# Kernel optimization log

Measured on AMD Instinct MI355X. Metric: run time of the kernel, lower is better.

## Reference

```python
import jax, jax.numpy as jnp
import numpy as np

B, T, N, D = 8, 512, 64, 128
PRED, HEADS, HID = 96, 8, 256
KERNELS = (17, 49)
NUM_LAYERS = 1
NUM_BLOCKS = 1
IDX_T = np.arange(64)   # lowest 64 of T//2=256 rfft modes (mode_select='low')
IDX_C = np.arange(32)   # min(modes, (N+1)//2)=32 lowest channel-frequency modes


def _mov_avg(x, k):
    # x: [B, T, N]; replicate-pad (k-1)//2 on both ends, then box filter (AvgPool1d stride 1)
    pad = (k - 1) // 2
    xp = jnp.concatenate([jnp.repeat(x[:, :1], pad, axis=1), x, jnp.repeat(x[:, -1:], pad, axis=1)], axis=1)
    c = jnp.cumsum(xp, axis=1)
    c = jnp.concatenate([jnp.zeros_like(c[:, :1]), c], axis=1)
    return (c[:, k:] - c[:, :-k]) / k


def _decomp_multi(x, dec_w, dec_b):
    # series_decomp_multi: softmax-weighted mixture of moving averages
    mm = jnp.stack([_mov_avg(x, k) for k in KERNELS], axis=-1)        # [B,T,N,K]
    w = jax.nn.softmax(x[..., None] * dec_w + dec_b, axis=-1)         # Linear(1,K) on x, softmax over K
    trend = jnp.sum(mm * w, axis=-1)
    return x - trend, trend


def _complex_attn(x, Wq, Wk, Wv, Wo):
    # x: complex64 [B, L, M, D]; multi-head attention over the M selected frequency modes.
    # Real projection weights applied to complex activations; attention weights are
    # softmax over |q k^H| / sqrt(dh); values stay complex.
    Bq, L, M, Dm = x.shape
    dh = Dm // HEADS
    q = jnp.einsum('blmd,de->blme', x, Wq).reshape(Bq, L, M, HEADS, dh)
    k = jnp.einsum('blmd,de->blme', x, Wk).reshape(Bq, L, M, HEADS, dh)
    v = jnp.einsum('blmd,de->blme', x, Wv).reshape(Bq, L, M, HEADS, dh)
    s = jnp.einsum('blmhd,blnhd->blhmn', q, jnp.conj(k))              # complex scores
    w = jax.nn.softmax(jnp.abs(s) / np.sqrt(dh), axis=-1)             # real attn weights
    o = jnp.einsum('blhmn,blnhd->blmhd', w.astype(x.dtype), v).reshape(Bq, L, M, Dm)
    return jnp.einsum('blmd,de->blme', o, Wo)


def _cem(x, Wq, Wk, Wv, Wo):
    # channel-frequency attention; x: [B, N, T, D]
    xp = jnp.transpose(x, (0, 2, 1, 3))                               # [B,T,N,D]
    xf = jnp.fft.rfft(xp, axis=2)                                     # [B,T,N//2+1,D]
    xs = xf[:, :, IDX_C, :]                                           # gather selected modes
    for _ in range(NUM_LAYERS):
        xs = _complex_attn(xs, Wq, Wk, Wv, Wo)
    yf = jnp.zeros((x.shape[0], T, N // 2 + 1, D), dtype=xf.dtype).at[:, :, IDX_C, :].set(xs)
    y = jnp.fft.irfft(yf, n=N, axis=2)
    return jnp.transpose(y, (0, 2, 1, 3))


def _tem(x, Wq, Wk, Wv, Wo):
    # temporal-frequency attention; x: [B, N, T, D]
    xf = jnp.fft.rfft(x, axis=2)                                      # [B,N,T//2+1,D]
    xs = xf[:, :, IDX_T, :]
    for _ in range(NUM_LAYERS):
        xs = _complex_attn(xs, Wq, Wk, Wv, Wo)
    yf = jnp.zeros((x.shape[0], N, T // 2 + 1, D), dtype=xf.dtype).at[:, :, IDX_T, :].set(xs)
    return jnp.fft.irfft(yf, n=T, axis=2)


def setup_inputs() -> dict:
    key = jax.random.key(0)
    ks = jax.random.split(key, 24)
    r = lambda i, shape, s: jax.random.normal(ks[i], shape, jnp.float32) * s
    K = len(KERNELS)
    return {
        'x': jax.random.normal(ks[0], (B, T, N), jnp.float32),
        'embeddings': jax.random.normal(ks[1], (1, D), jnp.float32),
        'dec_w': r(2, (K,), 1.0),
        'dec_b': jnp.zeros((K,), jnp.float32),
        'mlp_w1': r(3, (T, HID), 1.0 / np.sqrt(T)),
        'mlp_b1': jnp.zeros((HID,), jnp.float32),
        'mlp_w2': r(4, (HID, HID), 1.0 / np.sqrt(HID)),
        'mlp_b2': jnp.zeros((HID,), jnp.float32),
        'mlp_w3': r(5, (HID, PRED), 1.0 / np.sqrt(HID)),
        'mlp_b3': jnp.zeros((PRED,), jnp.float32),
        'cem_Wq': r(6, (D, D), 0.02), 'cem_Wk': r(7, (D, D), 0.02),
        'cem_Wv': r(8, (D, D), 0.02), 'cem_Wo': r(9, (D, D), 0.02),
        'tem_Wq': r(10, (D, D), 0.02), 'tem_Wk': r(11, (D, D), 0.02),
        'tem_Wv': r(12, (D, D), 0.02), 'tem_Wo': r(13, (D, D), 0.02),
        'dr_w': r(14, (D, 1), 1.0 / np.sqrt(D)),
        'dr_b': jnp.zeros((1,), jnp.float32),
        'out_w': r(15, (T, PRED), 1.0 / np.sqrt(T)),
        'out_b': jnp.zeros((PRED,), jnp.float32),
        'W_fuse': jnp.ones((2,), jnp.float32),
    }


def reference(x, embeddings, dec_w, dec_b, mlp_w1, mlp_b1, mlp_w2, mlp_b2, mlp_w3, mlp_b3,
              cem_Wq, cem_Wk, cem_Wv, cem_Wo, tem_Wq, tem_Wk, tem_Wv, tem_Wo,
              dr_w, dr_b, out_w, out_b, W_fuse):
    res, trend = _decomp_multi(x, dec_w, dec_b)
    t = jnp.transpose(trend, (0, 2, 1))                               # [B,N,T]
    h = jax.nn.relu(t @ mlp_w1 + mlp_b1)
    h = jax.nn.relu(h @ mlp_w2 + mlp_b2)
    trend_out = jnp.transpose(h @ mlp_w3 + mlp_b3, (0, 2, 1))         # [B,PRED,N]
    # tokenEmb: [B,T,N] -> [B,N,T,1] * [1,D]
    xe = jnp.transpose(res, (0, 2, 1))[..., None] * embeddings[0]      # [B,N,T,D]
    for _ in range(NUM_BLOCKS):
        xe = _cem(xe, cem_Wq, cem_Wk, cem_Wv, cem_Wo)
    for _ in range(NUM_BLOCKS):
        xe = _tem(xe, tem_Wq, tem_Wk, tem_Wv, tem_Wo)
    xr = jnp.einsum('bntd,do->bnto', xe, dr_w)[..., 0] + dr_b[0]      # dim_reduction -> [B,N,T]
    xo = jnp.transpose(jnp.einsum('bnt,tp->bnp', xr, out_w) + out_b, (0, 2, 1))  # [B,PRED,N]
    return W_fuse[0] * xo + W_fuse[1] * trend_out
```

## Files before the change

### kernel.cpp

```cpp
#include <hip/hip_runtime.h>
#include <hip/hip_bf16.h>

typedef __hip_bfloat16 bf16;
typedef float v2f __attribute__((ext_vector_type(2)));

constexpr int CB = 8;
constexpr int CT = 512;
constexpr int CN = 64;
constexpr int CD = 128;
constexpr int CP = 96;
constexpr int CH = 8;
constexpr int CDH = 16;
constexpr int CHID = 256;
constexpr int CM = 32;
constexpr int CG = 64;
constexpr float TWO_PI = 6.28318530717958647692f;

__device__ __forceinline__ float LD(const void* p, size_t i, bool f) {
  return f ? ((const float*)p)[i] : __bfloat162float(((const bf16*)p)[i]);
}
template <bool F32>
__device__ __forceinline__ float LDT(const void* p, size_t i) {
  return F32 ? ((const float*)p)[i] : __bfloat162float(((const bf16*)p)[i]);
}
__device__ __forceinline__ float b2f(short s) {
  return __uint_as_float(((unsigned int)(unsigned short)s) << 16);
}

__device__ __forceinline__ bool detect_f32(const void* x) {
  const unsigned int* xw = (const unsigned int*)x;
  unsigned int w = xw[threadIdx.x & 63];
  unsigned int e = (w >> 7) & 0xFF;
  unsigned long long m = __ballot(e >= 0x90 || e <= 0x60);
  return __popcll(m) > 3;
}

struct MArgs {
  const void *x, *dec_w, *dec_b, *out_w, *emb, *cWq, *cWk, *cWv, *cWo;
  const void *tWq, *tWk, *tWv, *tWo, *drw, *drb, *out_b, *wfuse;
  const void *w1, *b1, *w2, *b2, *w3, *b3;
  float *trendo, *Pbuf, *ewq, *ewk, *ewv, *wod, *owr, *owi, *chg;
  void* out;
};

__global__ __launch_bounds__(256, 4) void kPre(MArgs a) {
  __shared__ float sm[512];
  float* eml = sm;
  float* pp = sm + 128;
  float* prod = sm + 384;
  bool f32 = detect_f32(a.x);
  int tid = threadIdx.x;
  if (tid < 128) eml[tid] = LD(a.emb, tid, f32);
  __syncthreads();
  {
    int e = tid & 127, which = tid >> 7;
    const void* Wm = which ? a.cWk : a.cWq;
    float p = 0.f;
    #pragma unroll 8
    for (int d = 0; d < CD; ++d) p = fmaf(eml[d], LD(Wm, (size_t)d * CD + e, f32), p);
    pp[which * 128 + e] = p;
  }
  __syncthreads();
  if (tid < 128) prod[tid] = pp[tid] * pp[128 + tid];
  __syncthreads();
  if (tid < CH) {
    float s = 0.f;
    #pragma unroll
    for (int j = 0; j < 16; ++j) s += prod[tid * 16 + j];
    a.chg[tid] = fabsf(s);
  }
}

template <bool F32>
__device__ void k2_body(float* sm, const MArgs& a) {
  float* xbuf = sm;
  float* rows = sm;
  float* h1 = sm + 1536;
  float* h2 = sm + 2048;
  float* part = sm + 2560;
  int r0 = blockIdx.x * 2;
  int b = r0 >> 6, n0 = r0 & 63;
  int tid = threadIdx.x;
  size_t xb = (size_t)b * CT * CN + n0;
  for (int i = tid; i < CT * 2; i += 256) {
    int t = i >> 1, q = i & 1;
    xbuf[t * 3 + q] = LDT<F32>(a.x, xb + (size_t)t * CN + q);
  }
  __syncthreads();
  float trv[4];
  int q = tid & 1, tl = tid >> 1, t0 = tl * 4;
  {
    float w0 = LDT<F32>(a.dec_w, 0), w1 = LDT<F32>(a.dec_w, 1);
    float c0 = LDT<F32>(a.dec_b, 0), c1 = LDT<F32>(a.dec_b, 1);
    float s17 = 0.f, s49 = 0.f;
    #pragma unroll
    for (int o = -8; o <= 8; ++o) {
      int u = t0 + o; u = u < 0 ? 0 : (u > CT - 1 ? CT - 1 : u);
      s17 += xbuf[u * 3 + q];
    }
    #pragma unroll
    for (int o = -24; o <= 24; ++o) {
      int u = t0 + o; u = u < 0 ? 0 : (u > CT - 1 ? CT - 1 : u);
      s49 += xbuf[u * 3 + q];
    }
    #pragma unroll
    for (int k = 0; k < 4; ++k) {
      int t = t0 + k;
      if (k > 0) {
        int up8 = t + 8 > CT - 1 ? CT - 1 : t + 8;
        int dn9 = t - 9 < 0 ? 0 : t - 9;
        int up24 = t + 24 > CT - 1 ? CT - 1 : t + 24;
        int dn25 = t - 25 < 0 ? 0 : t - 25;
        s17 += xbuf[up8 * 3 + q] - xbuf[dn9 * 3 + q];
        s49 += xbuf[up24 * 3 + q] - xbuf[dn25 * 3 + q];
      }
      float m0 = s17 * (1.f / 17.f), m1 = s49 * (1.f / 49.f);
      float xv = xbuf[t * 3 + q];
      float l0 = xv * w0 + c0, l1 = xv * w1 + c1;
      float mx = fmaxf(l0, l1);
      float e0 = __expf(l0 - mx), e1 = __expf(l1 - mx);
      trv[k] = (e0 * m0 + e1 * m1) / (e0 + e1);
    }
  }
  __syncthreads();
  #pragma unroll
  for (int k = 0; k < 4; ++k) rows[q * CT + t0 + k] = trv[k];
  __syncthreads();
  int tt = tid >> 6, cq = tid & 63;
  {
    float ac0 = 0, ac1 = 0, ac2 = 0, ac3 = 0, ac4 = 0, ac5 = 0, ac6 = 0, ac7 = 0;
    int tg = tt * 128;
    if (F32) {
      const float4* w4 = (const float4*)a.w1;
      #pragma unroll 8
      for (int t = tg; t < tg + 128; ++t) {
        float4 wv = w4[t * 64 + cq];
        float rA = rows[t], rB = rows[CT + t];
        ac0 = fmaf(rA, wv.x, ac0); ac1 = fmaf(rA, wv.y, ac1);
        ac2 = fmaf(rA, wv.z, ac2); ac3 = fmaf(rA, wv.w, ac3);
        ac4 = fmaf(rB, wv.x, ac4); ac5 = fmaf(rB, wv.y, ac5);
        ac6 = fmaf(rB, wv.z, ac6); ac7 = fmaf(rB, wv.w, ac7);
      }
    } else {
      const short4* w4 = (const short4*)a.w1;
      #pragma unroll 8
      for (int t = tg; t < tg + 128; ++t) {
        short4 sv = w4[t * 64 + cq];
        float wx = b2f(sv.x), wy = b2f(sv.y), wz = b2f(sv.z), ww = b2f(sv.w);
        float rA = rows[t], rB = rows[CT + t];
        ac0 = fmaf(rA, wx, ac0); ac1 = fmaf(rA, wy, ac1);
        ac2 = fmaf(rA, wz, ac2); ac3 = fmaf(rA, ww, ac3);
        ac4 = fmaf(rB, wx, ac4); ac5 = fmaf(rB, wy, ac5);
        ac6 = fmaf(rB, wz, ac6); ac7 = fmaf(rB, ww, ac7);
      }
    }
    float4* pp = (float4*)(part + tt * 512 + cq * 4);
    pp[0] = make_float4(ac0, ac1, ac2, ac3);
    pp[64] = make_float4(ac4, ac5, ac6, ac7);
  }
  __syncthreads();
  {
    int c = tid;
    float bias = LDT<F32>(a.b1, c);
    float s0 = part[c] + part[512 + c] + part[1024 + c] + part[1536 + c];
    float s1 = part[256 + c] + part[768 + c] + part[1280 + c] + part[1792 + c];
    h1[c] = fmaxf(s0 + bias, 0.f);
    h1[CHID + c] = fmaxf(s1 + bias, 0.f);
  }
  __syncthreads();
  {
    float ac0 = 0, ac1 = 0, ac2 = 0, ac3 = 0, ac4 = 0, ac5 = 0, ac6 = 0, ac7 = 0;
    int ig = tt * 64;
    if (F32) {
      const float4* w4 = (const float4*)a.w2;
      #pragma unroll 8
      for (int i = ig; i < ig + 64; ++i) {
        float4 wv = w4[i * 64 + cq];
        float rA = h1[i], rB = h1[CHID + i];
        ac0 = fmaf(rA, wv.x, ac0); ac1 = fmaf(rA, wv.y, ac1);
        ac2 = fmaf(rA, wv.z, ac2); ac3 = fmaf(rA, wv.w, ac3);
        ac4 = fmaf(rB, wv.x, ac4); ac5 = fmaf(rB, wv.y, ac5);
        ac6 = fmaf(rB, wv.z, ac6); ac7 = fmaf(rB, wv.w, ac7);
      }
    } else {
      const short4* w4 = (const short4*)a.w2;
      #pragma unroll 8
      for (int i = ig; i < ig + 64; ++i) {
        short4 sv = w4[i * 64 + cq];
        float wx = b2f(sv.x), wy = b2f(sv.y), wz = b2f(sv.z), ww = b2f(sv.w);
        float rA = h1[i], rB = h1[CHID + i];
        ac0 = fmaf(rA, wx, ac0); ac1 = fmaf(rA, wy, ac1);
        ac2 = fmaf(rA, wz, ac2); ac3 = fmaf(rA, ww, ac3);
        ac4 = fmaf(rB, wx, ac4); ac5 = fmaf(rB, wy, ac5);
        ac6 = fmaf(rB, wz, ac6); ac7 = fmaf(rB, ww, ac7);
      }
    }
    float4* pp = (float4*)(part + tt * 512 + cq * 4);
    pp[0] = make_float4(ac0, ac1, ac2, ac3);
    pp[64] = make_float4(ac4, ac5, ac6, ac7);
  }
  __syncthreads();
  {
    int c = tid;
    float bias = LDT<F32>(a.b2, c);
    float s0 = part[c] + part[512 + c] + part[1024 + c] + part[1536 + c];
    float s1 = part[256 + c] + part[768 + c] + part[1280 + c] + part[1792 + c];
    h2[c] = fmaxf(s0 + bias, 0.f);
    h2[CHID + c] = fmaxf(s1 + bias, 0.f);
  }
  __syncthreads();
  if (tid < 2 * CP) {
    int p = tid < CP ? tid : tid - CP;
    int qh = tid < CP ? 0 : 1;
    float bias = LDT<F32>(a.b3, p);
    float a0 = 0.f;
    #pragma unroll 16
    for (int i = 0; i < CHID; ++i)
      a0 = fmaf(h2[qh * CHID + i], LDT<F32>(a.w3, i * CP + p), a0);
    a.trendo[((size_t)(b * CN + n0 + qh)) * CP + p] = a0 + bias;
  }
}

__global__ __launch_bounds__(256, 4) void kS2(MArgs a) {
  __shared__ __align__(16) float sm[4608];
  bool f32 = detect_f32(a.x);
  int blk = blockIdx.x, tid = threadIdx.x;
  if (blk < 256) {
    if (f32) k2_body<true>(sm, a);
    else     k2_body<false>(sm, a);
  } else if (blk < 1280) {
    float* xl = sm;
    float2* SL = (float2*)sm;
    float* rowl = sm + 3328;
    float* Rr = sm + 3584;
    float* Ri = sm + 3712;
    float* aR = sm + 3840;
    float* chl = sm + 4096;
    int bk = blk - 256;
    int b = bk >> 7, tbase = (bk & 127) * 4;
    int w = tid >> 6, lane = tid & 63;
    size_t xb = (size_t)b * CT * CN;
    for (int i = tid; i < 52 * 64; i += 256) {
      int r = i >> 6, n = i & 63;
      int u = tbase - 24 + r; u = u < 0 ? 0 : (u > CT - 1 ? CT - 1 : u);
      xl[i] = LD(a.x, xb + (size_t)u * CN + n, f32);
    }
    if (tid < CH) chl[tid] = a.chg[tid];
    __syncthreads();
    {
      int Lt = 24 + w;
      float w0 = LD(a.dec_w, 0, f32), w1 = LD(a.dec_w, 1, f32);
      float c0 = LD(a.dec_b, 0, f32), c1 = LD(a.dec_b, 1, f32);
      const float* xc = xl + Lt * 64 + lane;
      float pa = 0.f, pb = 0.f;
      #pragma unroll
      for (int o = -8; o <= 8; o += 2) pa += xc[o * 64];
      #pragma unroll
      for (int o = -7; o <= 7; o += 2) pb += xc[o * 64];
      float s17 = pa + pb;
      float qa = 0.f, qb = 0.f;
      #pragma unroll
      for (int o = 9; o <= 23; o += 2) qa += xc[o * 64] + xc[-o * 64];
      #pragma unroll
      for (int o = 10; o <= 24; o += 2) qb += xc[o * 64] + xc[-o * 64];
      float s49 = s17 + qa + qb;
      float m0 = s17 * (1.f / 17.f), m1 = s49 * (1.f / 49.f);
      float xv = xc[0];
      float l0 = xv * w0 + c0, l1 = xv * w1 + c1;
      float mx = fmaxf(l0, l1);
      float e0 = __expf(l0 - mx), e1 = __expf(l1 - mx);
      float tr = (e0 * m0 + e1 * m1) / (e0 + e1);
      rowl[w * 64 + lane] = xv - tr;
    }
    __syncthreads();
    float am, amax;
    {
      int m = lane & 31, half = lane >> 5;
      float cf, sf;
      sincosf((float)m * (TWO_PI / CN), &sf, &cf);
      float wr = (half & m & 1) ? -1.f : 1.f, wi = 0.f;
      float rr = 0.f, ri = 0.f;
      const float* rw = rowl + w * 64 + half * 32;
      #pragma unroll 8
      for (int j = 0; j < 32; ++j) {
        float xv = rw[j];
        rr = fmaf(xv, wr, rr);
        ri = fmaf(-xv, wi, ri);
        float nr = wr * cf - wi * sf; wi = wi * cf + wr * sf; wr = nr;
      }
      rr += __shfl_xor(rr, 32);
      ri += __shfl_xor(ri, 32);
      am = sqrtf(rr * rr + ri * ri);
      if (half == 0) { Rr[w * 32 + m] = rr; Ri[w * 32 + m] = ri; aR[w * 32 + m] = am; }
      amax = am;
      #pragma unroll
      for (int s2 = 1; s2 < 32; s2 <<= 1) amax = fmaxf(amax, __shfl_xor(amax, s2));
    }
    {
      float base2 = 0.25f * 1.44269504f * am;
      int hb = lane >> 5;
      float al0 = chl[hb] * base2;
      float al1 = chl[hb + 2] * base2;
      float al2 = chl[hb + 4] * base2;
      float al3 = chl[hb + 6] * base2;
      float den0 = 0, sr0 = 0, si0 = 0, den1 = 0, sr1 = 0, si1 = 0;
      float den2 = 0, sr2 = 0, si2 = 0, den3 = 0, sr3 = 0, si3 = 0;
      const float* aRw = aR + w * 32;
      const float* Rrw = Rr + w * 32;
      const float* Riw = Ri + w * 32;
      for (int n2 = 0; n2 < CM; ++n2) {
        float d = aRw[n2] - amax;
        float rrn = Rrw[n2], rin = Riw[n2];
        float e0 = exp2f(al0 * d); den0 += e0; sr0 = fmaf(e0, rrn, sr0); si0 = fmaf(e0, rin, si0);
        float e1 = exp2f(al1 * d); den1 += e1; sr1 = fmaf(e1, rrn, sr1); si1 = fmaf(e1, rin, si1);
        float e2 = exp2f(al2 * d); den2 += e2; sr2 = fmaf(e2, rrn, sr2); si2 = fmaf(e2, rin, si2);
        float e3 = exp2f(al3 * d); den3 += e3; sr3 = fmaf(e3, rrn, sr3); si3 = fmaf(e3, rin, si3);
      }
      float r0 = 1.f / den0, r1 = 1.f / den1, r2 = 1.f / den2, r3 = 1.f / den3;
      SL[w * 256 + lane      ] = make_float2(sr0 * r0, si0 * r0);
      SL[w * 256 + lane + 64 ] = make_float2(sr1 * r1, si1 * r1);
      SL[w * 256 + lane + 128] = make_float2(sr2 * r2, si2 * r2);
      SL[w * 256 + lane + 192] = make_float2(sr3 * r3, si3 * r3);
    }
    {
      int n2 = lane;
      const float2* Sw = SL + w * 256;
      float cd, sd;
      sincosf((float)n2 * (TWO_PI / CN), &sd, &cd);
      float c2 = cd * cd - sd * sd, s2 = 2.f * sd * cd;
      float pxA = 1.f, pyA = 0.f;
      float acc[8];
      #pragma unroll
      for (int h = 0; h < CH; ++h) acc[h] = -Sw[h * 32].x;
      for (int f2 = 0; f2 < 16; ++f2) {
        float pxB = pxA * cd - pyA * sd, pyB = pyA * cd + pxA * sd;
        float px2A = pxA + pxA, ny2A = -(pyA + pyA);
        float px2B = pxB + pxB, ny2B = -(pyB + pyB);
        #pragma unroll
        for (int h = 0; h < CH; ++h) {
          float4 sv = *(const float4*)(Sw + h * 32 + f2 * 2);
          acc[h] = fmaf(sv.x, px2A, acc[h]);
          acc[h] = fmaf(sv.y, ny2A, acc[h]);
          acc[h] = fmaf(sv.z, px2B, acc[h]);
          acc[h] = fmaf(sv.w, ny2B, acc[h]);
        }
        float nx = pxA * c2 - pyA * s2; pyA = pyA * c2 + pxA * s2; pxA = nx;
      }
      int t = tbase + w;
      float* Pb = a.Pbuf + (((size_t)(b * CN + n2)) * CT + t) * CH;
      ((float4*)Pb)[0] = make_float4(acc[0] * (1.f / CN), acc[1] * (1.f / CN),
                                     acc[2] * (1.f / CN), acc[3] * (1.f / CN));
      ((float4*)Pb)[1] = make_float4(acc[4] * (1.f / CN), acc[5] * (1.f / CN),
                                     acc[6] * (1.f / CN), acc[7] * (1.f / CN));
    }
  } else if (blk < 1344) {
    float* ps = sm;
    int g = blk - 1280;
    int tc = tid >> 7, idx = tid & 127;
    if (idx < CP) {
      int p = idx, t0 = tc * 256;
      float s0, c0v, ss, cs;
      sincosf((float)((g * t0) & (CT - 1)) * (TWO_PI / CT), &s0, &c0v);
      sincosf((float)g * (TWO_PI / CT), &ss, &cs);
      float wr = c0v, wi = s0, ar = 0.f, ai = 0.f;
      #pragma unroll 16
      for (int t = 0; t < 256; ++t) {
        float w = LD(a.out_w, (size_t)(t0 + t) * CP + p, f32);
        ar = fmaf(w, wr, ar); ai = fmaf(w, wi, ai);
        float nr = wr * cs - wi * ss; wi = wi * cs + wr * ss; wr = nr;
      }
      ps[(tc * CP + p) * 2] = ar; ps[(tc * CP + p) * 2 + 1] = ai;
    }
    __syncthreads();
    if (tid < CP) {
      a.owr[g * CP + tid] = ps[tid * 2] + ps[(CP + tid) * 2];
      a.owi[g * CP + tid] = ps[tid * 2 + 1] + ps[(CP + tid) * 2 + 1];
    }
  } else if (blk < 1356) {
    float* eml = sm;
    float* evl = sm + 128;
    float* ewoh = sm + 160;
    int bi = blk - 1344;
    int half = tid >> 7, e = tid & 127;
    int pairIdx = bi * 2 + half;
    int which = pairIdx >> 3, h = pairIdx & 7;
    if (tid < 128) eml[tid] = LD(a.emb, tid, f32);
    __syncthreads();
    if (e < 16) {
      float acc = 0;
      #pragma unroll 8
      for (int d = 0; d < CD; ++d) acc += eml[d] * LD(a.cWv, d * CD + h * CDH + e, f32);
      evl[half * 16 + e] = acc;
    }
    __syncthreads();
    {
      float acc = 0;
      #pragma unroll
      for (int j = 0; j < CDH; ++j)
        acc += evl[half * 16 + j] * LD(a.cWo, (h * CDH + j) * CD + e, f32);
      ewoh[half * 128 + e] = acc;
    }
    __syncthreads();
    {
      const void* W = which == 0 ? a.tWq : (which == 1 ? a.tWk : a.tWv);
      float acc = 0;
      #pragma unroll 8
      for (int d = 0; d < CD; ++d) acc += ewoh[half * 128 + d] * LD(W, d * CD + e, f32);
      (which == 0 ? a.ewq : (which == 1 ? a.ewk : a.ewv))[h * CD + e] = acc;
    }
  } else {
    float* drl = sm;
    if (tid < 128) drl[tid] = LD(a.drw, tid, f32);
    __syncthreads();
    if (tid < 128) {
      float acc = 0;
      #pragma unroll 8
      for (int d = 0; d < CD; ++d) acc += LD(a.tWo, tid * CD + d, f32) * drl[d];
      a.wod[tid] = acc;
    }
  }
}

__global__ __launch_bounds__(512, 4) void kC(MArgs a) {
  __shared__ __align__(16) float sm[13504];
  float* Pl = sm;
  float* QL = sm + 4352;
  float* Cl = sm + 5632;
  float* Ul = sm + 6144;
  float2* vdL = (float2*)(sm + 6208);
  float2* zL = (float2*)(sm + 7232);
  float* zrow = sm + 8256;
  float* Ab = sm + 8384;
  bool f32 = detect_f32(a.x);
  int blk = blockIdx.x, tid = threadIdx.x;
  int b = blk >> 6, n = blk & 63;
  const float4* src4 = (const float4*)(a.Pbuf + ((size_t)(b * CN + n)) * CT * CH);
  for (int i = tid; i < 1024; i += 512) {
    float4 v = src4[i];
    int t = i >> 1, half = i & 1;
    int k = t >> 6, u = t & 63;
    float* dst = Pl + u * 68 + half * 32 + k;
    dst[0] = v.x; dst[8] = v.y; dst[16] = v.z; dst[24] = v.w;
  }
  for (int id = tid; id < 512 + 64; id += 512) {
    if (id < 512) {
      int h = id >> 6, aa = (id >> 3) & 7, b2 = id & 7;
      float c = 0;
      #pragma unroll
      for (int j = 0; j < CDH; ++j)
        c += a.ewq[aa * CD + h * CDH + j] * a.ewk[b2 * CD + h * CDH + j];
      Cl[id] = c;
    } else {
      int r = id - 512;
      int h = r >> 3, aa = r & 7;
      float c = 0;
      #pragma unroll
      for (int j = 0; j < CDH; ++j) c += a.ewv[aa * CD + h * CDH + j] * a.wod[h * CDH + j];
      Ul[r] = c;
    }
  }
  __syncthreads();
  {
    int u = tid >> 3, h = tid & 7;
    const float* pr = Pl + u * 68 + h * 8;
    float p0 = pr[0], p1 = pr[1], p2 = pr[2], p3 = pr[3];
    float p4 = pr[4], p5 = pr[5], p6 = pr[6], p7 = pr[7];
    const float s = 0.70710678118654752f;
    float p04a = p0 + p4, p04s = p0 - p4;
    float p26a = p2 + p6, p26s = p2 - p6;
    float p17a = p1 + p7, p17s = p1 - p7;
    float p35a = p3 + p5, p35s = p3 - p5;
    float e1 = s * (p17a - p35a);
    float e2 = s * (p17s + p35s);
    float* ab = Ab + u * 80 + h * 10;
    ab[0] = p04a + p26a + p17a + p35a;
    ab[1] = 0.f;
    ab[2] = p04s + e1;
    ab[3] = -e2 - p26s;
    ab[4] = p04a - p26a;
    ab[5] = -(p17s - p35s);
    ab[6] = p04s - e1;
    ab[7] = -e2 + p26s;
    ab[8] = (p04a + p26a) - (p17a + p35a);
    ab[9] = 0.f;
  }
  __syncthreads();
  {
    int g = tid >> 3, h = tid & 7;
    int rho = g & 7;
    int rc = rho < 5 ? rho : 8 - rho;
    float ncsgn = rho < 5 ? -1.f : 1.f;
    float cs, sn;
    sincosf((float)g * (TWO_PI / CT), &sn, &cs);
    float cs2 = cs * cs - sn * sn, sn2 = 2.f * sn * cs;
    v2f wv0 = {1.f, 0.f};
    v2f wv1 = {cs, -sn};
    v2f qv0 = {0.f, 0.f}, qv1 = {0.f, 0.f};
    const float2* ab = (const float2*)(Ab + h * 10 + rc * 2);
    #pragma unroll 4
    for (int v = 0; v < 32; ++v) {
      float2 A0 = ab[v * 80];
      float2 A1 = ab[v * 80 + 40];
      float ar0 = A0.x, ni0 = ncsgn * A0.y;
      float ar1 = A1.x, ni1 = ncsgn * A1.y;
      v2f ws0 = {wv0.y, -wv0.x};
      v2f ws1 = {wv1.y, -wv1.x};
      qv0 += (v2f){ar0, ar0} * wv0;
      qv0 += (v2f){ni0, ni0} * ws0;
      qv1 += (v2f){ar1, ar1} * wv1;
      qv1 += (v2f){ni1, ni1} * ws1;
      wv0 = (v2f){cs2, cs2} * wv0 + (v2f){sn2, sn2} * ws0;
      wv1 = (v2f){cs2, cs2} * wv1 + (v2f){sn2, sn2} * ws1;
    }
    v2f qv = qv0 + qv1;
    QL[g * 20 + h * 2] = qv.x;
    QL[g * 20 + h * 2 + 1] = qv.y;
  }
  __syncthreads();
  int h = tid >> 6, m = tid & 63;
  v2f qp[8];
  {
    const float4* q4 = (const float4*)(QL + m * 20);
    #pragma unroll
    for (int j = 0; j < 4; ++j) {
      float4 qv = q4[j];
      qp[2 * j]     = (v2f){qv.x, qv.y};
      qp[2 * j + 1] = (v2f){qv.z, qv.w};
    }
  }
  {
    float vr = 0, vi = 0;
    #pragma unroll
    for (int aa = 0; aa < 8; ++aa) {
      float u = Ul[h * 8 + aa];
      vr = fmaf(qp[aa].x, u, vr); vi = fmaf(qp[aa].y, u, vi);
    }
    vdL[h * 64 + m] = make_float2(vr, vi);
  }
  v2f uu[8], vv[8];
  #pragma unroll
  for (int bb = 0; bb < 8; ++bb) {
    v2f acc = {0.f, 0.f};
    #pragma unroll
    for (int aa = 0; aa < 8; ++aa) acc += qp[aa] * Cl[(h * 8 + aa) * 8 + bb];
    uu[bb] = acc;
    vv[bb] = (v2f){acc.y, -acc.x};
  }
  float mx0 = -1e30f, den0 = 0.f, zr0 = 0.f, zi0 = 0.f;
  float mx1 = -1e30f, den1 = 0.f, zr1 = 0.f, zi1 = 0.f;
  #pragma unroll 4
  for (int gp = 0; gp < 32; ++gp) {
    {
      const float4* y4 = (const float4*)(QL + gp * 20);
      v2f sr2 = {0.f, 0.f}, si2 = {0.f, 0.f};
      #pragma unroll
      for (int j = 0; j < 4; ++j) {
        float4 yv = y4[j];
        v2f ya = {yv.x, yv.y}, yb = {yv.z, yv.w};
        sr2 = uu[2 * j] * ya + sr2;
        si2 = vv[2 * j] * ya + si2;
        sr2 = uu[2 * j + 1] * yb + sr2;
        si2 = vv[2 * j + 1] * yb + si2;
      }
      float sr = sr2.x + sr2.y;
      float si = si2.x + si2.y;
      float s = 0.25f * sqrtf(sr * sr + si * si);
      if (s > mx0) {
        float f = __expf(mx0 - s);
        den0 *= f; zr0 *= f; zi0 *= f; mx0 = s;
      }
      float e = __expf(s - mx0);
      float2 vd = vdL[h * 64 + gp];
      den0 += e; zr0 = fmaf(e, vd.x, zr0); zi0 = fmaf(e, vd.y, zi0);
    }
    {
      const float4* y4 = (const float4*)(QL + (gp + 32) * 20);
      v2f sr2 = {0.f, 0.f}, si2 = {0.f, 0.f};
      #pragma unroll
      for (int j = 0; j < 4; ++j) {
        float4 yv = y4[j];
        v2f ya = {yv.x, yv.y}, yb = {yv.z, yv.w};
        sr2 = uu[2 * j] * ya + sr2;
        si2 = vv[2 * j] * ya + si2;
        sr2 = uu[2 * j + 1] * yb + sr2;
        si2 = vv[2 * j + 1] * yb + si2;
      }
      float sr = sr2.x + sr2.y;
      float si = si2.x + si2.y;
      float s = 0.25f * sqrtf(sr * sr + si * si);
      if (s > mx1) {
        float f = __expf(mx1 - s);
        den1 *= f; zr1 *= f; zi1 *= f; mx1 = s;
      }
      float e = __expf(s - mx1);
      float2 vd = vdL[h * 64 + gp + 32];
      den1 += e; zr1 = fmaf(e, vd.x, zr1); zi1 = fmaf(e, vd.y, zi1);
    }
  }
  {
    float M = fmaxf(mx0, mx1);
    float ea = __expf(mx0 - M), eb = __expf(mx1 - M);
    float den = den0 * ea + den1 * eb;
    float zr = zr0 * ea + zr1 * eb;
    float zi = zi0 * ea + zi1 * eb;
    float rv = 1.f / den;
    zL[h * 64 + m] = make_float2(zr * rv, zi * rv);
  }
  __syncthreads();
  if (tid < 128) {
    int g = tid >> 1, c = tid & 1;
    float acc = 0;
    #pragma unroll
    for (int hh = 0; hh < CH; ++hh) acc += c ? zL[hh * 64 + g].y : zL[hh * 64 + g].x;
    zrow[g * 2 + c] = acc;
  }
  __syncthreads();
  if (tid < CP) {
    int p = tid;
    float acc = zrow[0] * a.owr[p] - zrow[1] * a.owi[p];
    #pragma unroll 8
    for (int g = 1; g < CG; ++g)
      acc += 2.f * (zrow[g * 2] * a.owr[g * CP + p] - zrow[g * 2 + 1] * a.owi[g * CP + p]);
    float xo = acc * (1.f / CT) + LD(a.drb, 0, f32) * a.owr[p] + LD(a.out_b, p, f32);
    float val = LD(a.wfuse, 0, f32) * xo
              + LD(a.wfuse, 1, f32) * a.trendo[((size_t)(b * CN + n)) * CP + p];
    size_t oidx = ((size_t)(b * CP + p)) * CN + n;
    if (f32) ((float*)a.out)[oidx] = val;
    else ((bf16*)a.out)[oidx] = __float2bfloat16(val);
  }
}

extern "C" void kernel_launch(void* const* d_in, const int* in_sizes, int n_in,
                              void* d_out, int out_size, void* d_ws, size_t ws_size,
                              hipStream_t stream) {
  float* W = (float*)d_ws;
  MArgs a;
  a.x = d_in[0];   a.emb = d_in[1];  a.dec_w = d_in[2]; a.dec_b = d_in[3];
  a.w1 = d_in[4];  a.b1 = d_in[5];   a.w2 = d_in[6];    a.b2 = d_in[7];
  a.w3 = d_in[8];  a.b3 = d_in[9];
  a.cWq = d_in[10]; a.cWk = d_in[11]; a.cWv = d_in[12]; a.cWo = d_in[13];
  a.tWq = d_in[14]; a.tWk = d_in[15]; a.tWv = d_in[16]; a.tWo = d_in[17];
  a.drw = d_in[18]; a.drb = d_in[19]; a.out_w = d_in[20]; a.out_b = d_in[21];
  a.wfuse = d_in[22];
  a.trendo = W; W += (size_t)CB * CN * CP;
  a.Pbuf = W;   W += (size_t)CB * CN * CT * CH;
  a.ewq = W;    W += CH * CD;
  a.ewk = W;    W += CH * CD;
  a.ewv = W;    W += CH * CD;
  a.wod = W;    W += CD;
  a.owr = W;    W += CG * CP;
  a.owi = W;    W += CG * CP;
  a.chg = W;    W += CH;
  a.out = d_out;

  kPre<<<1, 256, 0, stream>>>(a);
  kS2<<<1357, 256, 0, stream>>>(a);
  kC<<<512, 512, 0, stream>>>(a);
}
```

Baseline: 182.6 us.

## Split attention key range across wave halves, two queries per thread for LDS reuse

Each thread now handles two query modes (m and m+32) over half of the key modes, and the two halves of each 64-lane wave are merged with cross-lane shuffles of the online-softmax state. Every key row read from shared memory is therefore used for two queries instead of one, roughly halving LDS traffic in the score loop. In exchange it holds more registers per thread (two sets of projected queries and accumulators), adds a shuffle-based merge step, and drops the packed v2f arithmetic in favour of scalar FMAs.

```diff
diff --git a/kernel.cpp b/kernel.cpp
--- a/kernel.cpp
+++ b/kernel.cpp
@@ -517,94 +517,109 @@
     QL[g * 20 + h * 2 + 1] = qv.y;
   }
   __syncthreads();
-  int h = tid >> 6, m = tid & 63;
-  v2f qp[8];
-  {
-    const float4* q4 = (const float4*)(QL + m * 20);
-    #pragma unroll
-    for (int j = 0; j < 4; ++j) {
-      float4 qv = q4[j];
-      qp[2 * j]     = (v2f){qv.x, qv.y};
-      qp[2 * j + 1] = (v2f){qv.z, qv.w};
-    }
-  }
-  {
-    float vr = 0, vi = 0;
-    #pragma unroll
-    for (int aa = 0; aa < 8; ++aa) {
-      float u = Ul[h * 8 + aa];
-      vr = fmaf(qp[aa].x, u, vr); vi = fmaf(qp[aa].y, u, vi);
-    }
-    vdL[h * 64 + m] = make_float2(vr, vi);
-  }
-  v2f uu[8], vv[8];
-  #pragma unroll
-  for (int bb = 0; bb < 8; ++bb) {
-    v2f acc = {0.f, 0.f};
-    #pragma unroll
-    for (int aa = 0; aa < 8; ++aa) acc += qp[aa] * Cl[(h * 8 + aa) * 8 + bb];
-    uu[bb] = acc;
-    vv[bb] = (v2f){acc.y, -acc.x};
-  }
-  float mx0 = -1e30f, den0 = 0.f, zr0 = 0.f, zi0 = 0.f;
-  float mx1 = -1e30f, den1 = 0.f, zr1 = 0.f, zi1 = 0.f;
-  #pragma unroll 4
-  for (int gp = 0; gp < 32; ++gp) {
-    {
-      const float4* y4 = (const float4*)(QL + gp * 20);
-      v2f sr2 = {0.f, 0.f}, si2 = {0.f, 0.f};
+  {
+    int h = tid >> 6, lane = tid & 63;
+    int mb = lane & 31, kh = lane >> 5;
+    float uxA[8], uyA[8], uxB[8], uyB[8];
+    {
+      v2f qpA[8], qpB[8];
+      const float4* q4A = (const float4*)(QL + mb * 20);
+      const float4* q4B = (const float4*)(QL + (mb + 32) * 20);
+      #pragma unroll
+      for (int j = 0; j < 4; ++j) {
+        float4 qa = q4A[j], qb = q4B[j];
+        qpA[2 * j]     = (v2f){qa.x, qa.y};
+        qpA[2 * j + 1] = (v2f){qa.z, qa.w};
+        qpB[2 * j]     = (v2f){qb.x, qb.y};
+        qpB[2 * j + 1] = (v2f){qb.z, qb.w};
+      }
+      if (kh == 0) {
+        float vrA = 0, viA = 0, vrB = 0, viB = 0;
+        #pragma unroll
+        for (int aa = 0; aa < 8; ++aa) {
+          float u = Ul[h * 8 + aa];
+          vrA = fmaf(qpA[aa].x, u, vrA); viA = fmaf(qpA[aa].y, u, viA);
+          vrB = fmaf(qpB[aa].x, u, vrB); viB = fmaf(qpB[aa].y, u, viB);
+        }
+        vdL[h * 64 + mb]      = make_float2(vrA, viA);
+        vdL[h * 64 + mb + 32] = make_float2(vrB, viB);
+      }
+      #pragma unroll
+      for (int bb = 0; bb < 8; ++bb) {
+        float axA = 0, ayA = 0, axB = 0, ayB = 0;
+        #pragma unroll
+        for (int aa = 0; aa < 8; ++aa) {
+          float cl = Cl[(h * 8 + aa) * 8 + bb];
+          axA = fmaf(qpA[aa].x, cl, axA); ayA = fmaf(qpA[aa].y, cl, ayA);
+          axB = fmaf(qpB[aa].x, cl, axB); ayB = fmaf(qpB[aa].y, cl, ayB);
+        }
+        uxA[bb] = axA; uyA[bb] = ayA;
+        uxB[bb] = axB; uyB[bb] = ayB;
+      }
+    }
+    float mxA = -1e30f, denA = 0.f, zrA = 0.f, ziA = 0.f;
+    float mxB = -1e30f, denB = 0.f, zrB = 0.f, ziB = 0.f;
+    int g0 = kh * 32;
+    #pragma unroll 4
+    for (int gi = 0; gi < 32; ++gi) {
+      int g = g0 + gi;
+      const float4* y4 = (const float4*)(QL + g * 20);
+      float srA = 0, siA = 0, srB = 0, siB = 0;
       #pragma unroll
       for (int j = 0; j < 4; ++j) {
         float4 yv = y4[j];
-        v2f ya = {yv.x, yv.y}, yb = {yv.z, yv.w};
-        sr2 = uu[2 * j] * ya + sr2;
-        si2 = vv[2 * j] * ya + si2;
-        sr2 = uu[2 * j + 1] * yb + sr2;
-        si2 = vv[2 * j + 1] * yb + si2;
-      }
-      float sr = sr2.x + sr2.y;
-      float si = si2.x + si2.y;
-      float s = 0.25f * sqrtf(sr * sr + si * si);
-      if (s > mx0) {
-        float f = __expf(mx0 - s);
-        den0 *= f; zr0 *= f; zi0 *= f; mx0 = s;
-      }
-      float e = __expf(s - mx0);
-      float2 vd = vdL[h * 64 + gp];
-      den0 += e; zr0 = fmaf(e, vd.x, zr0); zi0 = fmaf(e, vd.y, zi0);
-    }
-    {
-      const float4* y4 = (const float4*)(QL + (gp + 32) * 20);
-      v2f sr2 = {0.f, 0.f}, si2 = {0.f, 0.f};
-      #pragma unroll
-      for (int j = 0; j < 4; ++j) {
-        float4 yv = y4[j];
-        v2f ya = {yv.x, yv.y}, yb = {yv.z, yv.w};
-        sr2 = uu[2 * j] * ya + sr2;
-        si2 = vv[2 * j] * ya + si2;
-        sr2 = uu[2 * j + 1] * yb + sr2;
-        si2 = vv[2 * j + 1] * yb + si2;
-      }
-      float sr = sr2.x + sr2.y;
-      float si = si2.x + si2.y;
-      float s = 0.25f * sqrtf(sr * sr + si * si);
-      if (s > mx1) {
-        float f = __expf(mx1 - s);
-        den1 *= f; zr1 *= f; zi1 *= f; mx1 = s;
-      }
-      float e = __expf(s - mx1);
-      float2 vd = vdL[h * 64 + gp + 32];
-      den1 += e; zr1 = fmaf(e, vd.x, zr1); zi1 = fmaf(e, vd.y, zi1);
-    }
-  }
-  {
-    float M = fmaxf(mx0, mx1);
-    float ea = __expf(mx0 - M), eb = __expf(mx1 - M);
-    float den = den0 * ea + den1 * eb;
-    float zr = zr0 * ea + zr1 * eb;
-    float zi = zi0 * ea + zi1 * eb;
-    float rv = 1.f / den;
-    zL[h * 64 + m] = make_float2(zr * rv, zi * rv);
+        int ja = 2 * j, jb = 2 * j + 1;
+        srA = fmaf(uxA[ja], yv.x, srA); srA = fmaf(uyA[ja], yv.y, srA);
+        siA = fmaf(uyA[ja], yv.x, siA); siA = fmaf(-uxA[ja], yv.y, siA);
+        srA = fmaf(uxA[jb], yv.z, srA); srA = fmaf(uyA[jb], yv.w, srA);
+        siA = fmaf(uyA[jb], yv.z, siA); siA = fmaf(-uxA[jb], yv.w, siA);
+        srB = fmaf(uxB[ja], yv.x, srB); srB = fmaf(uyB[ja], yv.y, srB);
+        siB = fmaf(uyB[ja], yv.x, siB); siB = fmaf(-uxB[ja], yv.y, siB);
+        srB = fmaf(uxB[jb], yv.z, srB); srB = fmaf(uyB[jb], yv.w, srB);
+        siB = fmaf(uyB[jb], yv.z, siB); siB = fmaf(-uxB[jb], yv.w, siB);
+      }
+      float sA = 0.25f * sqrtf(srA * srA + siA * siA);
+      float sB = 0.25f * sqrtf(srB * srB + siB * siB);
+      float2 vd = vdL[h * 64 + g];
+      if (sA > mxA) {
+        float f = __expf(mxA - sA);
+        denA *= f; zrA *= f; ziA *= f; mxA = sA;
+      }
+      float eA = __expf(sA - mxA);
+      denA += eA; zrA = fmaf(eA, vd.x, zrA); ziA = fmaf(eA, vd.y, ziA);
+      if (sB > mxB) {
+        float f = __expf(mxB - sB);
+        denB *= f; zrB *= f; ziB *= f; mxB = sB;
+      }
+      float eB = __expf(sB - mxB);
+      denB += eB; zrB = fmaf(eB, vd.x, zrB); ziB = fmaf(eB, vd.y, ziB);
+    }
+    {
+      float mx2 = __shfl_xor(mxA, 32), den2 = __shfl_xor(denA, 32);
+      float zr2 = __shfl_xor(zrA, 32), zi2 = __shfl_xor(ziA, 32);
+      float M = fmaxf(mxA, mx2);
+      float ea = __expf(mxA - M), eb = __expf(mx2 - M);
+      float den = denA * ea + den2 * eb;
+      float zr = zrA * ea + zr2 * eb;
+      float zi = ziA * ea + zi2 * eb;
+      if (kh == 0) {
+        float rv = 1.f / den;
+        zL[h * 64 + mb] = make_float2(zr * rv, zi * rv);
+      }
+    }
+    {
+      float mx2 = __shfl_xor(mxB, 32), den2 = __shfl_xor(denB, 32);
+      float zr2 = __shfl_xor(zrB, 32), zi2 = __shfl_xor(ziB, 32);
+      float M = fmaxf(mxB, mx2);
+      float ea = __expf(mxB - M), eb = __expf(mx2 - M);
+      float den = denB * ea + den2 * eb;
+      float zr = zrB * ea + zr2 * eb;
+      float zi = ziB * ea + zi2 * eb;
+      if (kh == 0) {
+        float rv = 1.f / den;
+        zL[h * 64 + mb + 32] = make_float2(zr * rv, zi * rv);
+      }
+    }
   }
   __syncthreads();
   if (tid < 128) {
```

After: 184.9 us. About the same (+1.3%).

## Move trend MLP into pre-kernel and reuse residual from global buffer

Applied to the files above, without the earlier changes.

The one-block kPre kernel is merged with the trend-MLP blocks into a new kernel kA. Those blocks now also write the decomposition residual to a new global buffer. kS2's channel-FFT blocks read that residual directly instead of reloading a 52-row window of x and recomputing the moving-average decomposition. This removes redundant decomposition work and halo loads, in exchange for an extra 1 MB global write/read and the MLP work now being serialized before kS2 rather than overlapping with it.

```diff
diff --git a/kernel.cpp b/kernel.cpp
--- a/kernel.cpp
+++ b/kernel.cpp
@@ -39,46 +39,17 @@
   const void *x, *dec_w, *dec_b, *out_w, *emb, *cWq, *cWk, *cWv, *cWo;
   const void *tWq, *tWk, *tWv, *tWo, *drw, *drb, *out_b, *wfuse;
   const void *w1, *b1, *w2, *b2, *w3, *b3;
-  float *trendo, *Pbuf, *ewq, *ewk, *ewv, *wod, *owr, *owi, *chg;
+  float *trendo, *Pbuf, *ewq, *ewk, *ewv, *wod, *owr, *owi, *chg, *res;
   void* out;
 };
 
-__global__ __launch_bounds__(256, 4) void kPre(MArgs a) {
-  __shared__ float sm[512];
-  float* eml = sm;
-  float* pp = sm + 128;
-  float* prod = sm + 384;
-  bool f32 = detect_f32(a.x);
-  int tid = threadIdx.x;
-  if (tid < 128) eml[tid] = LD(a.emb, tid, f32);
-  __syncthreads();
-  {
-    int e = tid & 127, which = tid >> 7;
-    const void* Wm = which ? a.cWk : a.cWq;
-    float p = 0.f;
-    #pragma unroll 8
-    for (int d = 0; d < CD; ++d) p = fmaf(eml[d], LD(Wm, (size_t)d * CD + e, f32), p);
-    pp[which * 128 + e] = p;
-  }
-  __syncthreads();
-  if (tid < 128) prod[tid] = pp[tid] * pp[128 + tid];
-  __syncthreads();
-  if (tid < CH) {
-    float s = 0.f;
-    #pragma unroll
-    for (int j = 0; j < 16; ++j) s += prod[tid * 16 + j];
-    a.chg[tid] = fabsf(s);
-  }
-}
-
 template <bool F32>
-__device__ void k2_body(float* sm, const MArgs& a) {
+__device__ void k2_body(float* sm, const MArgs& a, int r0) {
   float* xbuf = sm;
   float* rows = sm;
   float* h1 = sm + 1536;
   float* h2 = sm + 2048;
   float* part = sm + 2560;
-  int r0 = blockIdx.x * 2;
   int b = r0 >> 6, n0 = r0 & 63;
   int tid = threadIdx.x;
   size_t xb = (size_t)b * CT * CN + n0;
@@ -120,6 +91,7 @@
       float mx = fmaxf(l0, l1);
       float e0 = __expf(l0 - mx), e1 = __expf(l1 - mx);
       trv[k] = (e0 * m0 + e1 * m1) / (e0 + e1);
+      a.res[((size_t)b * CT + t) * CN + n0 + q] = xv - trv[k];
     }
   }
   __syncthreads();
@@ -221,57 +193,55 @@
   }
 }
 
+__global__ __launch_bounds__(256, 4) void kA(MArgs a) {
+  __shared__ __align__(16) float sm[4608];
+  bool f32 = detect_f32(a.x);
+  int tid = threadIdx.x;
+  if (blockIdx.x == 0) {
+    float* eml = sm;
+    float* pp = sm + 128;
+    float* prod = sm + 384;
+    if (tid < 128) eml[tid] = LD(a.emb, tid, f32);
+    __syncthreads();
+    {
+      int e = tid & 127, which = tid >> 7;
+      const void* Wm = which ? a.cWk : a.cWq;
+      float p = 0.f;
+      #pragma unroll 8
+      for (int d = 0; d < CD; ++d) p = fmaf(eml[d], LD(Wm, (size_t)d * CD + e, f32), p);
+      pp[which * 128 + e] = p;
+    }
+    __syncthreads();
+    if (tid < 128) prod[tid] = pp[tid] * pp[128 + tid];
+    __syncthreads();
+    if (tid < CH) {
+      float s = 0.f;
+      #pragma unroll
+      for (int j = 0; j < 16; ++j) s += prod[tid * 16 + j];
+      a.chg[tid] = fabsf(s);
+    }
+  } else {
+    int r0 = (blockIdx.x - 1) * 2;
+    if (f32) k2_body<true>(sm, a, r0);
+    else     k2_body<false>(sm, a, r0);
+  }
+}
+
 __global__ __launch_bounds__(256, 4) void kS2(MArgs a) {
   __shared__ __align__(16) float sm[4608];
   bool f32 = detect_f32(a.x);
   int blk = blockIdx.x, tid = threadIdx.x;
-  if (blk < 256) {
-    if (f32) k2_body<true>(sm, a);
-    else     k2_body<false>(sm, a);
-  } else if (blk < 1280) {
-    float* xl = sm;
-    float2* SL = (float2*)sm;
-    float* rowl = sm + 3328;
-    float* Rr = sm + 3584;
-    float* Ri = sm + 3712;
-    float* aR = sm + 3840;
-    float* chl = sm + 4096;
-    int bk = blk - 256;
-    int b = bk >> 7, tbase = (bk & 127) * 4;
+  if (blk < 1024) {
+    float* rowl = sm;
+    float* Rr = sm + 256;
+    float* Ri = sm + 384;
+    float* aR = sm + 512;
+    float* chl = sm + 640;
+    float2* SL = (float2*)(sm + 648);
+    int b = blk >> 7, tbase = (blk & 127) * 4;
     int w = tid >> 6, lane = tid & 63;
-    size_t xb = (size_t)b * CT * CN;
-    for (int i = tid; i < 52 * 64; i += 256) {
-      int r = i >> 6, n = i & 63;
-      int u = tbase - 24 + r; u = u < 0 ? 0 : (u > CT - 1 ? CT - 1 : u);
-      xl[i] = LD(a.x, xb + (size_t)u * CN + n, f32);
-    }
+    rowl[tid] = a.res[((size_t)(b * CT + tbase + w)) * CN + lane];
     if (tid < CH) chl[tid] = a.chg[tid];
-    __syncthreads();
-    {
-      int Lt = 24 + w;
-      float w0 = LD(a.dec_w, 0, f32), w1 = LD(a.dec_w, 1, f32);
-      float c0 = LD(a.dec_b, 0, f32), c1 = LD(a.dec_b, 1, f32);
-      const float* xc = xl + Lt * 64 + lane;
-      float pa = 0.f, pb = 0.f;
-      #pragma unroll
-      for (int o = -8; o <= 8; o += 2) pa += xc[o * 64];
-      #pragma unroll
-      for (int o = -7; o <= 7; o += 2) pb += xc[o * 64];
-      float s17 = pa + pb;
-      float qa = 0.f, qb = 0.f;
-      #pragma unroll
-      for (int o = 9; o <= 23; o += 2) qa += xc[o * 64] + xc[-o * 64];
-      #pragma unroll
-      for (int o = 10; o <= 24; o += 2) qb += xc[o * 64] + xc[-o * 64];
-      float s49 = s17 + qa + qb;
-      float m0 = s17 * (1.f / 17.f), m1 = s49 * (1.f / 49.f);
-      float xv = xc[0];
-      float l0 = xv * w0 + c0, l1 = xv * w1 + c1;
-      float mx = fmaxf(l0, l1);
-      float e0 = __expf(l0 - mx), e1 = __expf(l1 - mx);
-      float tr = (e0 * m0 + e1 * m1) / (e0 + e1);
-      rowl[w * 64 + lane] = xv - tr;
-    }
     __syncthreads();
     float am, amax;
     {
@@ -353,9 +323,9 @@
       ((float4*)Pb)[1] = make_float4(acc[4] * (1.f / CN), acc[5] * (1.f / CN),
                                      acc[6] * (1.f / CN), acc[7] * (1.f / CN));
     }
-  } else if (blk < 1344) {
+  } else if (blk < 1088) {
     float* ps = sm;
-    int g = blk - 1280;
+    int g = blk - 1024;
     int tc = tid >> 7, idx = tid & 127;
     if (idx < CP) {
       int p = idx, t0 = tc * 256;
@@ -376,11 +346,11 @@
       a.owr[g * CP + tid] = ps[tid * 2] + ps[(CP + tid) * 2];
       a.owi[g * CP + tid] = ps[tid * 2 + 1] + ps[(CP + tid) * 2 + 1];
     }
-  } else if (blk < 1356) {
+  } else if (blk < 1100) {
     float* eml = sm;
     float* evl = sm + 128;
     float* ewoh = sm + 160;
-    int bi = blk - 1344;
+    int bi = blk - 1088;
     int half = tid >> 7, e = tid & 127;
     int pairIdx = bi * 2 + half;
     int which = pairIdx >> 3, h = pairIdx & 7;
@@ -651,9 +621,10 @@
   a.owr = W;    W += CG * CP;
   a.owi = W;    W += CG * CP;
   a.chg = W;    W += CH;
+  a.res = W;    W += (size_t)CB * CT * CN;
   a.out = d_out;
 
-  kPre<<<1, 256, 0, stream>>>(a);
-  kS2<<<1357, 256, 0, stream>>>(a);
+  kA<<<257, 256, 0, stream>>>(a);
+  kS2<<<1101, 256, 0, stream>>>(a);
   kC<<<512, 512, 0, stream>>>(a);
 }
```

Result: slower. 191.7 us (+5.0%).
